# Kernel tuning notes

Measured on AMD Instinct MI355X. Metric: run time of the kernel, lower is better.

Reference implementation:

```python
import jax, jax.numpy as jnp
import numpy as np

KINEMATIC_CHAIN = [[0, 2, 5, 8, 11], [0, 1, 4, 7, 10], [0, 3, 6, 9, 12, 15],
                   [9, 14, 17, 19, 21], [9, 13, 16, 18, 20]]
PATHS = [c[1:] for c in KINEMATIC_CHAIN]  # paths = chain[1:] per gauss_integral_motion
FRAMES, JOINTS = 16384, 22


def setup_inputs() -> dict:
    key = jax.random.key(0)
    k1, k2 = jax.random.split(key)
    motion1 = jax.random.normal(k1, (FRAMES, JOINTS, 3), dtype=jnp.float32)
    motion2 = jax.random.normal(k2, (FRAMES, JOINTS, 3), dtype=jnp.float32)
    return {"motion1": motion1, "motion2": motion2}


def _safe_normalize(v):
    # vec / norm(vec) if norm != 0 else zeros  (matches the torch list comp)
    n = jnp.linalg.norm(v, axis=-1, keepdims=True)
    return jnp.where(n > 0, v / jnp.where(n > 0, n, 1.0), 0.0)


def _gli_pair(p1, p2):
    """Sum of Gauss link integrals over all segment pairs of two paths.
    p1: (L1, 3), p2: (L2, 3) -> scalar. Vectorized over the (L1-1, L2-1) segment grid."""
    s1, e1 = p1[:-1, None, :], p1[1:, None, :]   # (n1, 1, 3)
    s2, e2 = p2[None, :-1, :], p2[None, 1:, :]   # (1, n2, 3)
    r13, r14 = s2 - s1, e2 - s1
    r23, r24 = s2 - e1, e2 - e1
    r12, r34 = e1 - s1, e2 - s2
    faces = [jnp.cross(r13, r14), jnp.cross(r14, r24),
             jnp.cross(r24, r23), jnp.cross(r23, r13)]
    nf = [_safe_normalize(f) for f in faces]
    gli = jnp.zeros(jnp.broadcast_shapes(r13.shape[:-1], r24.shape[:-1]), p1.dtype)
    for i in range(4):
        d = jnp.clip(jnp.sum(nf[i] * nf[(i + 1) % 4], axis=-1), -1.0, 1.0)
        gli = gli + jnp.arcsin(d)
    sign = jnp.sum(jnp.cross(r34, r12) * r13, axis=-1)
    gli = gli * jnp.where(sign > 0, 1.0, -1.0) / (4.0 * jnp.pi)
    return jnp.sum(gli)


def _window_mask(motion1, motion2):
    # xz bounding-box overlap per frame, then dilate each contiguous run by 1
    # frame on each side (start = count-1, end = count+1-1 in the torch code).
    def bbox(m):  # (F, J, 3) -> min/max over joints of x and z
        x, z = m[..., 0], m[..., 2]
        return x.min(1), x.max(1), z.min(1), z.max(1)
    x1n, x1x, z1n, z1x = bbox(motion1)
    x2n, x2x, z2n, z2x = bbox(motion2)
    ov_x = ~((x1x < x2n) | (x2x < x1n))
    ov_z = ~((z1x < z2n) | (z2x < z1n))
    f = ov_x & ov_z  # (F,) bool
    false1 = jnp.zeros((1,), dtype=bool)
    prev = jnp.concatenate([false1, f[:-1]])
    nxt = jnp.concatenate([f[1:], false1])
    return f | prev | nxt


def _gli_motion(motion1, motion2):
    frame = motion1.shape[0]
    n_paths = len(PATHS)
    mask = _window_mask(motion1, motion2).astype(motion1.dtype)  # (F,)
    # GLI_motion[i, a, b]: vmap each path-pair over frames (25 fixed pairs)
    rows = []
    for pa in PATHS:
        p1 = motion1[:, jnp.asarray(pa), :]  # (F, La, 3)
        cols = []
        for pb in PATHS:
            p2 = motion2[:, jnp.asarray(pb), :]  # (F, Lb, 3)
            cols.append(jax.vmap(_gli_pair)(p1, p2))  # (F,)
        rows.append(jnp.stack(cols, axis=-1))  # (F, n_paths)
    gli = jnp.stack(rows, axis=-2)  # (F, n_paths, n_paths)
    gli = gli * mask[:, None, None]  # frames outside windows stay zero
    vel = jnp.abs(gli[1:] - gli[:-1]).reshape(frame - 1, n_paths * n_paths)
    return jnp.max(vel, axis=1)  # (F-1,)


def reference(motion1, motion2):
    return _gli_motion(motion1, motion2)
```

## Files before the change

### kernel.cpp

```cpp
#include <hip/hip_runtime.h>
#include <math.h>

#define NFRAMES 16384
#define NJOINTS 22
#define NPATHS  5
#define NPAIRS  (NPATHS * NPATHS)
#define NSEG    16
#define GSTRIDE 32
#define FSTR    (NJOINTS * 3)
#define FPB     4

typedef float v4f __attribute__((ext_vector_type(4)));

__constant__ int2 c_seg[NSEG] = {
    {6,15},{15,24},{24,33},
    {3,12},{12,21},{21,30},
    {9,18},{18,27},{27,36},{36,45},
    {42,51},{51,57},{57,63},
    {39,48},{48,54},{54,60}
};
__constant__ int c_pstart[NPATHS] = {0, 3, 6, 10, 13};
__constant__ int c_plen[NPATHS]   = {3, 3, 4, 3, 3};

struct V3 { v4f x, y, z; };
__device__ __forceinline__ V3 vsub(V3 a, V3 b) { V3 r; r.x=a.x-b.x; r.y=a.y-b.y; r.z=a.z-b.z; return r; }
__device__ __forceinline__ v4f vdot(V3 a, V3 b) { return a.x*b.x + a.y*b.y + a.z*b.z; }
__device__ __forceinline__ V3 vcross(V3 a, V3 b) {
    V3 r;
    r.x = a.y*b.z - a.z*b.y;
    r.y = a.z*b.x - a.x*b.z;
    r.z = a.x*b.y - a.y*b.x;
    return r;
}

__device__ __forceinline__ v4f vasin_term(v4f d, v4f m) {
    v4f rs;
#pragma unroll
    for (int i = 0; i < 4; i++) rs[i] = __builtin_amdgcn_rsqf(m[i]);
    v4f x = d * rs;
    v4f one = 1.0f;
    v4f a = __builtin_elementwise_max(x, -x);
    a = __builtin_elementwise_min(a, one);
    v4f p = a * -0.0187293f + 0.0742610f;
    p = a * p + -0.2121144f;
    p = a * p + 1.5707288f;
    v4f om = one - a;
    v4f s;
#pragma unroll
    for (int i = 0; i < 4; i++) s[i] = __builtin_amdgcn_sqrtf(om[i]);
    v4f r = 1.5707963268f - s * p;
#pragma unroll
    for (int i = 0; i < 4; i++) {
        float ri = (x[i] < 0.0f) ? -r[i] : r[i];
        r[i] = (m[i] > 0.0f) ? ri : 0.0f;
    }
    return r;
}

__device__ __forceinline__ v4f shfl_xor_v4(v4f v, int mask, int width) {
    v4f r;
#pragma unroll
    for (int i = 0; i < 4; i++) r[i] = __shfl_xor(v[i], mask, width);
    return r;
}

__global__ __launch_bounds__(64, 2) void k_gli(const float* __restrict__ m1,
                                               const float* __restrict__ m2,
                                               float* __restrict__ gli,
                                               int* __restrict__ ov) {
    __shared__ v4f sF[2 * FSTR];
    __shared__ v4f sT[260];

    int l = threadIdx.x;
    int fp = blockIdx.x * FPB;
    const float* a = m1 + (size_t)fp * FSTR;
    const float* b = m2 + (size_t)fp * FSTR;

    int j = l & 15;
    int i0 = l >> 4;
    int2 o2 = c_seg[j];
    int2 o1s[4];
#pragma unroll
    for (int k = 0; k < 4; k++) o1s[k] = c_seg[i0 + 4 * k];

    {
        v4f va, vb;
#pragma unroll
        for (int r = 0; r < 4; r++) { va[r] = a[r * FSTR + l]; vb[r] = b[r * FSTR + l]; }
        sF[l] = va;
        sF[FSTR + l] = vb;
        if (l < FSTR - 64) {
            int co = 64 + l;
            v4f wa, wb;
#pragma unroll
            for (int r = 0; r < 4; r++) { wa[r] = a[r * FSTR + co]; wb[r] = b[r * FSTR + co]; }
            sF[co] = wa;
            sF[FSTR + co] = wb;
        }
        if (l == 32) sT[256] = v4f{0.0f, 0.0f, 0.0f, 0.0f};
    }
    __syncthreads();

    {
        int half = l >> 5;
        int jj = l & 31;
        if (jj > NJOINTS - 1) jj = NJOINTS - 1;
        const v4f* p = sF + half * FSTR;
        v4f x = p[jj * 3 + 0];
        v4f z = p[jj * 3 + 2];
        v4f xn = x, xx = x, zn = z, zx = z;
#pragma unroll
        for (int k = 1; k < 32; k <<= 1) {
            xn = __builtin_elementwise_min(xn, shfl_xor_v4(xn, k, 32));
            xx = __builtin_elementwise_max(xx, shfl_xor_v4(xx, k, 32));
            zn = __builtin_elementwise_min(zn, shfl_xor_v4(zn, k, 32));
            zx = __builtin_elementwise_max(zx, shfl_xor_v4(zx, k, 32));
        }
        v4f oxn = shfl_xor_v4(xn, 32, 64);
        v4f oxx = shfl_xor_v4(xx, 32, 64);
        v4f ozn = shfl_xor_v4(zn, 32, 64);
        v4f ozx = shfl_xor_v4(zx, 32, 64);
        if (l == 0) {
            int4 o;
            int res[4];
#pragma unroll
            for (int r = 0; r < 4; r++) {
                bool vx = !((xx[r] < oxn[r]) || (oxx[r] < xn[r]));
                bool vz = !((zx[r] < ozn[r]) || (ozx[r] < zn[r]));
                res[r] = (vx && vz) ? 1 : 0;
            }
            o.x = res[0]; o.y = res[1]; o.z = res[2]; o.w = res[3];
            *(int4*)(ov + fp) = o;
        }
    }

    {
        const v4f* B = sF + FSTR;
        V3 s2; s2.x = B[o2.x]; s2.y = B[o2.x+1]; s2.z = B[o2.x+2];
        V3 e2; e2.x = B[o2.y]; e2.y = B[o2.y+1]; e2.z = B[o2.y+2];
#pragma unroll
        for (int k = 0; k < 4; k++) {
            int2 o1 = o1s[k];
            V3 s1; s1.x = sF[o1.x]; s1.y = sF[o1.x+1]; s1.z = sF[o1.x+2];
            V3 e1; e1.x = sF[o1.y]; e1.y = sF[o1.y+1]; e1.z = sF[o1.y+2];

            V3 r12 = vsub(e1, s1);
            V3 r13 = vsub(s2, s1);
            V3 r14 = vsub(e2, s1);

            V3 f0v = vcross(r13, r14);
            V3 c1  = vcross(r12, r13);
            V3 c2  = vcross(r12, r14);
            v4f sg = -vdot(c2, r13);
            V3 f2  = vsub(vsub(c2, c1), f0v);

            v4f q0 = vdot(f0v, f0v);
            v4f q1 = vdot(c2, c2);
            v4f q2 = vdot(f2, f2);
            v4f q3 = vdot(c1, c1);
            v4f d0 =  vdot(f0v, c2);
            v4f d1 =  vdot(c2, f2);
            v4f d2 = -vdot(f2, c1);
            v4f d3 = -vdot(c1, f0v);

            v4f g = vasin_term(d0, q0 * q1)
                  + vasin_term(d1, q1 * q2)
                  + vasin_term(d2, q2 * q3)
                  + vasin_term(d3, q3 * q0);

            v4f res;
#pragma unroll
            for (int r = 0; r < 4; r++) res[r] = (sg[r] > 0.0f) ? g[r] : -g[r];
            sT[l + 64 * k] = res;
        }
    }
    __syncthreads();

    if (l < NPAIRS) {
        int pa = (l * 205) >> 10;
        int pb = l - pa * 5;
        int ia0 = c_pstart[pa], na = c_plen[pa];
        int ib0 = c_pstart[pb], nb = c_plen[pb];
        v4f s = v4f{0.0f, 0.0f, 0.0f, 0.0f};
#pragma unroll
        for (int ka = 0; ka < 4; ka++) {
#pragma unroll
            for (int kb = 0; kb < 4; kb++) {
                int idx = (ka < na && kb < nb) ? ((ia0 + ka) * 16 + (ib0 + kb)) : 256;
                s += sT[idx];
            }
        }
        s *= 0.07957747154594767f;
#pragma unroll
        for (int r = 0; r < 4; r++)
            gli[(size_t)(fp + r) * GSTRIDE + l] = s[r];
    }
}

__global__ void k_out(const float* __restrict__ gli, const int* __restrict__ ov,
                      float* __restrict__ out) {
    int f = blockIdx.x * blockDim.x + threadIdx.x;
    if (f >= NFRAMES - 1) return;

    int m0 = ov[f];
    if (f > 0) m0 |= ov[f - 1];
    m0 |= ov[f + 1];

    int m1 = ov[f + 1] | ov[f];
    if (f + 2 <= NFRAMES - 1) m1 |= ov[f + 2];

    float ma = m0 ? 1.0f : 0.0f;
    float mb = m1 ? 1.0f : 0.0f;

    const float4* g0v = (const float4*)(gli + (size_t)f * GSTRIDE);
    const float4* g1v = (const float4*)(gli + (size_t)(f + 1) * GSTRIDE);
    float v = 0.0f;
#pragma unroll
    for (int q = 0; q < 6; q++) {
        float4 u0 = g0v[q];
        float4 u1 = g1v[q];
        v = fmaxf(v, fabsf(u1.x * mb - u0.x * ma));
        v = fmaxf(v, fabsf(u1.y * mb - u0.y * ma));
        v = fmaxf(v, fabsf(u1.z * mb - u0.z * ma));
        v = fmaxf(v, fabsf(u1.w * mb - u0.w * ma));
    }
    {
        float u0 = ((const float*)g0v)[24];
        float u1 = ((const float*)g1v)[24];
        v = fmaxf(v, fabsf(u1 * mb - u0 * ma));
    }
    out[f] = v;
}

extern "C" void kernel_launch(void* const* d_in, const int* in_sizes, int n_in,
                              void* d_out, int out_size, void* d_ws, size_t ws_size,
                              hipStream_t stream) {
    const float* m1 = (const float*)d_in[0];
    const float* m2 = (const float*)d_in[1];
    float* out = (float*)d_out;

    float* gli = (float*)d_ws;
    int* ov = (int*)(gli + (size_t)NFRAMES * GSTRIDE);

    k_gli<<<NFRAMES / FPB, 64, 0, stream>>>(m1, m2, gli, ov);

    {
        int threads = 256;
        int blocks = (NFRAMES - 1 + threads - 1) / threads;
        k_out<<<blocks, threads, 0, stream>>>(gli, ov, out);
    }
}
```

Measured before the change: 79.01 us.

## Fuse GLI computation and velocity-max output into one kernel with halo frames

```diff
diff --git a/kernel.cpp b/kernel.cpp
--- a/kernel.cpp
+++ b/kernel.cpp
@@ -6,9 +6,8 @@
 #define NPATHS  5
 #define NPAIRS  (NPATHS * NPATHS)
 #define NSEG    16
-#define GSTRIDE 32
 #define FSTR    (NJOINTS * 3)
-#define FPB     4
+#define FPB     8
 
 typedef float v4f __attribute__((ext_vector_type(4)));
 
@@ -57,6 +56,25 @@
     return r;
 }
 
+struct S3 { float x, y, z; };
+__device__ __forceinline__ S3 ssub(S3 a, S3 b) { return S3{a.x-b.x, a.y-b.y, a.z-b.z}; }
+__device__ __forceinline__ float sdot(S3 a, S3 b) { return fmaf(a.x, b.x, fmaf(a.y, b.y, a.z*b.z)); }
+__device__ __forceinline__ S3 scross(S3 a, S3 b) {
+    return S3{ fmaf(a.y, b.z, -a.z*b.y), fmaf(a.z, b.x, -a.x*b.z), fmaf(a.x, b.y, -a.y*b.x) };
+}
+__device__ __forceinline__ float asin_term_s(float d, float m) {
+    float rs = __builtin_amdgcn_rsqf(m);
+    float x = d * rs;
+    float a = fminf(fabsf(x), 1.0f);
+    float p = fmaf(a, -0.0187293f, 0.0742610f);
+    p = fmaf(a, p, -0.2121144f);
+    p = fmaf(a, p, 1.5707288f);
+    float s = __builtin_amdgcn_sqrtf(1.0f - a);
+    float r = fmaf(-s, p, 1.5707963268f);
+    r = (x < 0.0f) ? -r : r;
+    return (m > 0.0f) ? r : 0.0f;
+}
+
 __device__ __forceinline__ v4f shfl_xor_v4(v4f v, int mask, int width) {
     v4f r;
 #pragma unroll
@@ -64,172 +82,247 @@
     return r;
 }
 
-__global__ __launch_bounds__(64, 2) void k_gli(const float* __restrict__ m1,
-                                               const float* __restrict__ m2,
-                                               float* __restrict__ gli,
-                                               int* __restrict__ ov) {
-    __shared__ v4f sF[2 * FSTR];
-    __shared__ v4f sT[260];
+__device__ __forceinline__ int bbox4(v4f x, v4f z, int l) {
+    v4f xn = x, xx = x, zn = z, zx = z;
+#pragma unroll
+    for (int k = 1; k < 32; k <<= 1) {
+        xn = __builtin_elementwise_min(xn, shfl_xor_v4(xn, k, 32));
+        xx = __builtin_elementwise_max(xx, shfl_xor_v4(xx, k, 32));
+        zn = __builtin_elementwise_min(zn, shfl_xor_v4(zn, k, 32));
+        zx = __builtin_elementwise_max(zx, shfl_xor_v4(zx, k, 32));
+    }
+    v4f oxn = shfl_xor_v4(xn, 32, 64);
+    v4f oxx = shfl_xor_v4(xx, 32, 64);
+    v4f ozn = shfl_xor_v4(zn, 32, 64);
+    v4f ozx = shfl_xor_v4(zx, 32, 64);
+    int bits = 0;
+    if (l == 0) {
+#pragma unroll
+        for (int r = 0; r < 4; r++) {
+            bool vx = !((xx[r] < oxn[r]) || (oxx[r] < xn[r]));
+            bool vz = !((zx[r] < ozn[r]) || (ozx[r] < zn[r]));
+            if (vx && vz) bits |= 1 << r;
+        }
+    }
+    return bits;
+}
+
+__device__ __forceinline__ void gli_terms_v4(const v4f* sF, v4f* sT, int l,
+                                             int2 o2, const int2* o1s) {
+    const v4f* B = sF + FSTR;
+    V3 s2; s2.x = B[o2.x]; s2.y = B[o2.x+1]; s2.z = B[o2.x+2];
+    V3 e2; e2.x = B[o2.y]; e2.y = B[o2.y+1]; e2.z = B[o2.y+2];
+#pragma unroll
+    for (int k = 0; k < 4; k++) {
+        int2 o1 = o1s[k];
+        V3 s1; s1.x = sF[o1.x]; s1.y = sF[o1.x+1]; s1.z = sF[o1.x+2];
+        V3 e1; e1.x = sF[o1.y]; e1.y = sF[o1.y+1]; e1.z = sF[o1.y+2];
+
+        V3 r12 = vsub(e1, s1);
+        V3 r13 = vsub(s2, s1);
+        V3 r14 = vsub(e2, s1);
+
+        V3 f0v = vcross(r13, r14);
+        V3 c1  = vcross(r12, r13);
+        V3 c2  = vcross(r12, r14);
+        v4f sg = -vdot(c2, r13);
+        V3 f2  = vsub(vsub(c2, c1), f0v);
+
+        v4f q0 = vdot(f0v, f0v);
+        v4f q1 = vdot(c2, c2);
+        v4f q2 = vdot(f2, f2);
+        v4f q3 = vdot(c1, c1);
+        v4f d0 =  vdot(f0v, c2);
+        v4f d1 =  vdot(c2, f2);
+        v4f d2 = -vdot(f2, c1);
+        v4f d3 = -vdot(c1, f0v);
+
+        v4f g = vasin_term(d0, q0 * q1)
+              + vasin_term(d1, q1 * q2)
+              + vasin_term(d2, q2 * q3)
+              + vasin_term(d3, q3 * q0);
+
+        v4f res;
+#pragma unroll
+        for (int r = 0; r < 4; r++) res[r] = (sg[r] > 0.0f) ? g[r] : -g[r];
+        sT[l + 64 * k] = res;
+    }
+}
+
+__device__ __forceinline__ void gli_terms_s(const float* sF, float* sT, int l,
+                                            int2 o2, const int2* o1s) {
+    const float* B = sF + FSTR;
+    S3 s2{B[o2.x], B[o2.x+1], B[o2.x+2]};
+    S3 e2{B[o2.y], B[o2.y+1], B[o2.y+2]};
+#pragma unroll
+    for (int k = 0; k < 4; k++) {
+        int2 o1 = o1s[k];
+        S3 s1{sF[o1.x], sF[o1.x+1], sF[o1.x+2]};
+        S3 e1{sF[o1.y], sF[o1.y+1], sF[o1.y+2]};
+        S3 r12 = ssub(e1, s1), r13 = ssub(s2, s1), r14 = ssub(e2, s1);
+        S3 f0v = scross(r13, r14), c1 = scross(r12, r13), c2 = scross(r12, r14);
+        float sg = -sdot(c2, r13);
+        S3 f2 = ssub(ssub(c2, c1), f0v);
+        float q0 = sdot(f0v, f0v), q1 = sdot(c2, c2), q2 = sdot(f2, f2), q3 = sdot(c1, c1);
+        float d0 = sdot(f0v, c2), d1 = sdot(c2, f2), d2 = -sdot(f2, c1), d3 = -sdot(c1, f0v);
+        float g = asin_term_s(d0, q0*q1) + asin_term_s(d1, q1*q2)
+                + asin_term_s(d2, q2*q3) + asin_term_s(d3, q3*q0);
+        sT[l + 64*k] = (sg > 0.0f) ? g : -g;
+    }
+}
+
+__device__ __forceinline__ v4f bin_reduce_v4(const v4f* sT, int ia0, int na, int ib0, int nb) {
+    v4f s = v4f{0.0f, 0.0f, 0.0f, 0.0f};
+#pragma unroll
+    for (int ka = 0; ka < 4; ka++)
+#pragma unroll
+        for (int kb = 0; kb < 4; kb++) {
+            int idx = (ka < na && kb < nb) ? ((ia0 + ka) * 16 + (ib0 + kb)) : 256;
+            s += sT[idx];
+        }
+    return s * 0.07957747154594767f;
+}
+__device__ __forceinline__ float bin_reduce_s(const float* sT, int ia0, int na, int ib0, int nb) {
+    float s = 0.0f;
+#pragma unroll
+    for (int ka = 0; ka < 4; ka++)
+#pragma unroll
+        for (int kb = 0; kb < 4; kb++) {
+            int idx = (ka < na && kb < nb) ? ((ia0 + ka) * 16 + (ib0 + kb)) : 256;
+            s += sT[idx];
+        }
+    return s * 0.07957747154594767f;
+}
+
+__device__ __forceinline__ void stage4(const float* src, v4f* dst, int l) {
+    v4f v;
+#pragma unroll
+    for (int r = 0; r < 4; r++) v[r] = src[r * FSTR + l];
+    dst[l] = v;
+    if (l < FSTR - 64) {
+        int co = 64 + l;
+        v4f w;
+#pragma unroll
+        for (int r = 0; r < 4; r++) w[r] = src[r * FSTR + co];
+        dst[co] = w;
+    }
+}
+
+__global__ __launch_bounds__(64, 2) void k_fused(const float* __restrict__ m1,
+                                                 const float* __restrict__ m2,
+                                                 float* __restrict__ out) {
+    __shared__ v4f   sF4a[2 * FSTR];
+    __shared__ v4f   sF4b[2 * FSTR];
+    __shared__ float sFh[2 * FSTR];
+    __shared__ v4f   sT4[260];
+    __shared__ float sTh[260];
 
     int l = threadIdx.x;
-    int fp = blockIdx.x * FPB;
-    const float* a = m1 + (size_t)fp * FSTR;
-    const float* b = m2 + (size_t)fp * FSTR;
-
-    int j = l & 15;
+    int F = blockIdx.x * FPB;
+    const float* a = m1 + (size_t)F * FSTR;
+    const float* b = m2 + (size_t)F * FSTR;
+
+    int jseg = l & 15;
     int i0 = l >> 4;
-    int2 o2 = c_seg[j];
+    int2 o2 = c_seg[jseg];
     int2 o1s[4];
 #pragma unroll
     for (int k = 0; k < 4; k++) o1s[k] = c_seg[i0 + 4 * k];
 
-    {
-        v4f va, vb;
-#pragma unroll
-        for (int r = 0; r < 4; r++) { va[r] = a[r * FSTR + l]; vb[r] = b[r * FSTR + l]; }
-        sF[l] = va;
-        sF[FSTR + l] = vb;
-        if (l < FSTR - 64) {
-            int co = 64 + l;
-            v4f wa, wb;
-#pragma unroll
-            for (int r = 0; r < 4; r++) { wa[r] = a[r * FSTR + co]; wb[r] = b[r * FSTR + co]; }
-            sF[co] = wa;
-            sF[FSTR + co] = wb;
-        }
-        if (l == 32) sT[256] = v4f{0.0f, 0.0f, 0.0f, 0.0f};
-    }
-    __syncthreads();
-
-    {
-        int half = l >> 5;
-        int jj = l & 31;
-        if (jj > NJOINTS - 1) jj = NJOINTS - 1;
-        const v4f* p = sF + half * FSTR;
-        v4f x = p[jj * 3 + 0];
-        v4f z = p[jj * 3 + 2];
-        v4f xn = x, xx = x, zn = z, zx = z;
-#pragma unroll
-        for (int k = 1; k < 32; k <<= 1) {
-            xn = __builtin_elementwise_min(xn, shfl_xor_v4(xn, k, 32));
-            xx = __builtin_elementwise_max(xx, shfl_xor_v4(xx, k, 32));
-            zn = __builtin_elementwise_min(zn, shfl_xor_v4(zn, k, 32));
-            zx = __builtin_elementwise_max(zx, shfl_xor_v4(zx, k, 32));
-        }
-        v4f oxn = shfl_xor_v4(xn, 32, 64);
-        v4f oxx = shfl_xor_v4(xx, 32, 64);
-        v4f ozn = shfl_xor_v4(zn, 32, 64);
-        v4f ozx = shfl_xor_v4(zx, 32, 64);
-        if (l == 0) {
-            int4 o;
-            int res[4];
-#pragma unroll
-            for (int r = 0; r < 4; r++) {
-                bool vx = !((xx[r] < oxn[r]) || (oxx[r] < xn[r]));
-                bool vz = !((zx[r] < ozn[r]) || (ozx[r] < zn[r]));
-                res[r] = (vx && vz) ? 1 : 0;
-            }
-            o.x = res[0]; o.y = res[1]; o.z = res[2]; o.w = res[3];
-            *(int4*)(ov + fp) = o;
-        }
-    }
-
-    {
-        const v4f* B = sF + FSTR;
-        V3 s2; s2.x = B[o2.x]; s2.y = B[o2.x+1]; s2.z = B[o2.x+2];
-        V3 e2; e2.x = B[o2.y]; e2.y = B[o2.y+1]; e2.z = B[o2.y+2];
-#pragma unroll
-        for (int k = 0; k < 4; k++) {
-            int2 o1 = o1s[k];
-            V3 s1; s1.x = sF[o1.x]; s1.y = sF[o1.x+1]; s1.z = sF[o1.x+2];
-            V3 e1; e1.x = sF[o1.y]; e1.y = sF[o1.y+1]; e1.z = sF[o1.y+2];
-
-            V3 r12 = vsub(e1, s1);
-            V3 r13 = vsub(s2, s1);
-            V3 r14 = vsub(e2, s1);
-
-            V3 f0v = vcross(r13, r14);
-            V3 c1  = vcross(r12, r13);
-            V3 c2  = vcross(r12, r14);
-            v4f sg = -vdot(c2, r13);
-            V3 f2  = vsub(vsub(c2, c1), f0v);
-
-            v4f q0 = vdot(f0v, f0v);
-            v4f q1 = vdot(c2, c2);
-            v4f q2 = vdot(f2, f2);
-            v4f q3 = vdot(c1, c1);
-            v4f d0 =  vdot(f0v, c2);
-            v4f d1 =  vdot(c2, f2);
-            v4f d2 = -vdot(f2, c1);
-            v4f d3 = -vdot(c1, f0v);
-
-            v4f g = vasin_term(d0, q0 * q1)
-                  + vasin_term(d1, q1 * q2)
-                  + vasin_term(d2, q2 * q3)
-                  + vasin_term(d3, q3 * q0);
-
-            v4f res;
-#pragma unroll
-            for (int r = 0; r < 4; r++) res[r] = (sg[r] > 0.0f) ? g[r] : -g[r];
-            sT[l + 64 * k] = res;
-        }
-    }
-    __syncthreads();
-
+    int ia0 = 0, na = 0, ib0 = 0, nb = 0;
     if (l < NPAIRS) {
         int pa = (l * 205) >> 10;
         int pb = l - pa * 5;
-        int ia0 = c_pstart[pa], na = c_plen[pa];
-        int ib0 = c_pstart[pb], nb = c_plen[pb];
-        v4f s = v4f{0.0f, 0.0f, 0.0f, 0.0f};
-#pragma unroll
-        for (int ka = 0; ka < 4; ka++) {
-#pragma unroll
-            for (int kb = 0; kb < 4; kb++) {
-                int idx = (ka < na && kb < nb) ? ((ia0 + ka) * 16 + (ib0 + kb)) : 256;
-                s += sT[idx];
-            }
-        }
-        s *= 0.07957747154594767f;
-#pragma unroll
-        for (int r = 0; r < 4; r++)
-            gli[(size_t)(fp + r) * GSTRIDE + l] = s[r];
-    }
-}
-
-__global__ void k_out(const float* __restrict__ gli, const int* __restrict__ ov,
-                      float* __restrict__ out) {
-    int f = blockIdx.x * blockDim.x + threadIdx.x;
-    if (f >= NFRAMES - 1) return;
-
-    int m0 = ov[f];
-    if (f > 0) m0 |= ov[f - 1];
-    m0 |= ov[f + 1];
-
-    int m1 = ov[f + 1] | ov[f];
-    if (f + 2 <= NFRAMES - 1) m1 |= ov[f + 2];
-
-    float ma = m0 ? 1.0f : 0.0f;
-    float mb = m1 ? 1.0f : 0.0f;
-
-    const float4* g0v = (const float4*)(gli + (size_t)f * GSTRIDE);
-    const float4* g1v = (const float4*)(gli + (size_t)(f + 1) * GSTRIDE);
-    float v = 0.0f;
-#pragma unroll
-    for (int q = 0; q < 6; q++) {
-        float4 u0 = g0v[q];
-        float4 u1 = g1v[q];
-        v = fmaxf(v, fabsf(u1.x * mb - u0.x * ma));
-        v = fmaxf(v, fabsf(u1.y * mb - u0.y * ma));
-        v = fmaxf(v, fabsf(u1.z * mb - u0.z * ma));
-        v = fmaxf(v, fabsf(u1.w * mb - u0.w * ma));
-    }
+        ia0 = c_pstart[pa]; na = c_plen[pa];
+        ib0 = c_pstart[pb]; nb = c_plen[pb];
+    }
+
+    stage4(a, sF4a, l);
+    stage4(b, sF4a + FSTR, l);
+    stage4(a + 4 * FSTR, sF4b, l);
+    stage4(b + 4 * FSTR, sF4b + FSTR, l);
     {
-        float u0 = ((const float*)g0v)[24];
-        float u1 = ((const float*)g1v)[24];
-        v = fmaxf(v, fabsf(u1 * mb - u0 * ma));
-    }
-    out[f] = v;
+        int hf = F + 8; if (hf > NFRAMES - 1) hf = NFRAMES - 1;
+        const float* ah = m1 + (size_t)hf * FSTR;
+        const float* bh = m2 + (size_t)hf * FSTR;
+        sFh[l] = ah[l];
+        sFh[FSTR + l] = bh[l];
+        if (l < FSTR - 64) {
+            sFh[64 + l] = ah[64 + l];
+            sFh[FSTR + 64 + l] = bh[64 + l];
+        }
+    }
+    if (l == 32) sT4[256] = v4f{0.0f, 0.0f, 0.0f, 0.0f};
+    if (l == 33) sTh[256] = 0.0f;
+    __syncthreads();
+
+    int half = l >> 5;
+    int jj = l & 31; if (jj > NJOINTS - 1) jj = NJOINTS - 1;
+    int ovbits = 0;
+    {
+        const v4f* p = sF4a + half * FSTR;
+        ovbits |= bbox4(p[jj*3 + 0], p[jj*3 + 2], l) << 1;
+    }
+    {
+        const v4f* p = sF4b + half * FSTR;
+        ovbits |= bbox4(p[jj*3 + 0], p[jj*3 + 2], l) << 5;
+    }
+    {
+        const float* gb = half ? m2 : m1;
+        int fm1 = (F > 0) ? F - 1 : 0;
+        int fp9 = F + 9; if (fp9 > NFRAMES - 1) fp9 = NFRAMES - 1;
+        float xm1 = gb[(size_t)fm1 * FSTR + jj*3];
+        float zm1 = gb[(size_t)fm1 * FSTR + jj*3 + 2];
+        float x8  = sFh[half * FSTR + jj*3];
+        float z8  = sFh[half * FSTR + jj*3 + 2];
+        float x9  = gb[(size_t)fp9 * FSTR + jj*3];
+        float z9  = gb[(size_t)fp9 * FSTR + jj*3 + 2];
+        v4f x{xm1, x8, x9, x8};
+        v4f z{zm1, z8, z9, z8};
+        int bc = bbox4(x, z, l);
+        if (l == 0) {
+            if (F > 0                 && (bc & 1)) ovbits |= 1 << 0;
+            if (F + 8 <= NFRAMES - 1  && (bc & 2)) ovbits |= 1 << 9;
+            if (F + 9 <= NFRAMES - 1  && (bc & 4)) ovbits |= 1 << 10;
+        }
+    }
+
+    gli_terms_v4(sF4a, sT4, l, o2, o1s);
+    __syncthreads();
+    v4f gA = bin_reduce_v4(sT4, ia0, na, ib0, nb);
+    __syncthreads();
+    gli_terms_v4(sF4b, sT4, l, o2, o1s);
+    gli_terms_s(sFh, sTh, l, o2, o1s);
+    __syncthreads();
+    v4f gB = bin_reduce_v4(sT4, ia0, na, ib0, nb);
+    float gh = bin_reduce_s(sTh, ia0, na, ib0, nb);
+
+    ovbits = __shfl(ovbits, 0, 64);
+    float mk[9];
+#pragma unroll
+    for (int r = 0; r < 9; r++) mk[r] = ((ovbits >> r) & 7) ? 1.0f : 0.0f;
+    float g[9];
+#pragma unroll
+    for (int r = 0; r < 4; r++) { g[r] = gA[r]; g[4 + r] = gB[r]; }
+    g[8] = gh;
+    float d[8];
+#pragma unroll
+    for (int r = 0; r < 8; r++) d[r] = fabsf(g[r + 1] * mk[r + 1] - g[r] * mk[r]);
+#pragma unroll
+    for (int k = 1; k < 64; k <<= 1) {
+#pragma unroll
+        for (int r = 0; r < 8; r++) d[r] = fmaxf(d[r], __shfl_xor(d[r], k, 64));
+    }
+    if (l == 0) {
+        *(float4*)(out + F) = float4{d[0], d[1], d[2], d[3]};
+        if (F + FPB < NFRAMES) {
+            *(float4*)(out + F + 4) = float4{d[4], d[5], d[6], d[7]};
+        } else {
+            out[F + 4] = d[4];
+            out[F + 5] = d[5];
+            out[F + 6] = d[6];
+        }
+    }
 }
 
 extern "C" void kernel_launch(void* const* d_in, const int* in_sizes, int n_in,
@@ -238,15 +331,7 @@
     const float* m1 = (const float*)d_in[0];
     const float* m2 = (const float*)d_in[1];
     float* out = (float*)d_out;
-
-    float* gli = (float*)d_ws;
-    int* ov = (int*)(gli + (size_t)NFRAMES * GSTRIDE);
-
-    k_gli<<<NFRAMES / FPB, 64, 0, stream>>>(m1, m2, gli, ov);
-
-    {
-        int threads = 256;
-        int blocks = (NFRAMES - 1 + threads - 1) / threads;
-        k_out<<<blocks, threads, 0, stream>>>(gli, ov, out);
-    }
-}
+    (void)d_ws; (void)ws_size;
+
+    k_fused<<<NFRAMES / FPB, 64, 0, stream>>>(m1, m2, out);
+}
```

Measured after the change: 83.48 us. 5.7% more time.
